# Performance work log

Measured on AMD Instinct MI355X. Metric: run time of the kernel, lower is better.

## Reference

```python
import jax, jax.numpy as jnp
import numpy as np

NEG_BIG = 1e8  # mask value from the original code


def setup_inputs() -> dict:
    key = jax.random.key(0)
    k1, k2, k3, k4, k5 = jax.random.split(key, 5)
    B, L, H, D = 16, 128, 256, 256
    # xavier-uniform-ish scale for the weight matrices
    lim = float(np.sqrt(6.0 / (H + D)))
    return {
        "encoder_output": jax.random.normal(k1, (B, L, H), dtype=jnp.float32),
        "W_l": jax.random.uniform(k2, (H, D), jnp.float32, -lim, lim),
        "W_r": jax.random.uniform(k3, (H, D), jnp.float32, -lim, lim),
        "U": jax.random.uniform(k4, (D,), jnp.float32, 0.0, 1.0),
        "logit_bias": jax.random.uniform(k5, (1,), jnp.float32, 0.0, 1.0),
    }


def reference(encoder_output, W_l, W_r, U, logit_bias):
    B, L, H = encoder_output.shape
    # projections: (B, L, D)
    dot_l = jnp.einsum("blh,hd->bld", encoder_output, W_l)
    dot_r = jnp.einsum("blh,hd->bld", encoder_output, W_r)
    # pairwise additive attention: (B, L, L, D) -> (B, L, L)
    final_sum = jnp.tanh(dot_l[:, :, None, :] + dot_r[:, None, :, :])
    logits = jnp.einsum("bijd,d->bij", final_sum, U) + logit_bias[0]
    # per-step diagonal mask (one_hot(i) at step i) vectorized as eye
    mask = jnp.eye(L, dtype=logits.dtype)  # (L, L)
    mask_scores = logits - NEG_BIG * mask[None, :, :]  # (B, L, L)
    probs = jax.nn.sigmoid(mask_scores)
    # Bernoulli sample (fixed key for reproducibility)
    samples = jax.random.bernoulli(jax.random.key(1), probs).astype(logits.dtype)  # graphs (B,L,L)
    # Bernoulli entropy: p*softplus(-l) + (1-p)*softplus(l), numerically stable
    entropy = probs * jax.nn.softplus(-mask_scores) + (1.0 - probs) * jax.nn.softplus(mask_scores)
    graph_batch = jnp.mean(samples, axis=0)  # (L, L)
    # BCE-with-logits mean over all elements (targets = sampled graphs)
    log_softmax = jnp.mean(jax.nn.softplus(mask_scores) - mask_scores * samples)
    entropy_regularization = jnp.mean(jnp.mean(entropy, axis=2), axis=1)  # (B,)
    return (mask_scores, samples, entropy, graph_batch, log_softmax, entropy_regularization)
```

## Files before the change

### kernel.cpp

```cpp
#include <hip/hip_runtime.h>

#define Bn 16
#define Ln 128
#define Hn 256
#define Dn 256

#define OFF_MASK   0
#define OFF_SMP    262144
#define OFF_ENT    524288
#define OFF_GRAPH  786432
#define OFF_LSE    802816
#define OFF_EREG   802817

static __device__ __forceinline__ unsigned rotl32(unsigned x, int r) {
  return (x << r) | (x >> (32 - r));
}

static __device__ __forceinline__ unsigned threefry_bits(unsigned c_hi, unsigned c_lo) {
  const unsigned ks0 = 0u, ks1 = 1u;
  const unsigned ks2 = 0u ^ 1u ^ 0x1BD11BDAu;
  unsigned x0 = c_hi + ks0;
  unsigned x1 = c_lo + ks1;
  x0 += x1; x1 = rotl32(x1, 13); x1 ^= x0;
  x0 += x1; x1 = rotl32(x1, 15); x1 ^= x0;
  x0 += x1; x1 = rotl32(x1, 26); x1 ^= x0;
  x0 += x1; x1 = rotl32(x1, 6);  x1 ^= x0;
  x0 += ks1; x1 += ks2 + 1u;
  x0 += x1; x1 = rotl32(x1, 17); x1 ^= x0;
  x0 += x1; x1 = rotl32(x1, 29); x1 ^= x0;
  x0 += x1; x1 = rotl32(x1, 16); x1 ^= x0;
  x0 += x1; x1 = rotl32(x1, 24); x1 ^= x0;
  x0 += ks2; x1 += ks0 + 2u;
  x0 += x1; x1 = rotl32(x1, 13); x1 ^= x0;
  x0 += x1; x1 = rotl32(x1, 15); x1 ^= x0;
  x0 += x1; x1 = rotl32(x1, 26); x1 ^= x0;
  x0 += x1; x1 = rotl32(x1, 6);  x1 ^= x0;
  x0 += ks0; x1 += ks1 + 3u;
  x0 += x1; x1 = rotl32(x1, 17); x1 ^= x0;
  x0 += x1; x1 = rotl32(x1, 29); x1 ^= x0;
  x0 += x1; x1 = rotl32(x1, 16); x1 ^= x0;
  x0 += x1; x1 = rotl32(x1, 24); x1 ^= x0;
  x0 += ks1; x1 += ks2 + 4u;
  x0 += x1; x1 = rotl32(x1, 13); x1 ^= x0;
  x0 += x1; x1 = rotl32(x1, 15); x1 ^= x0;
  x0 += x1; x1 = rotl32(x1, 26); x1 ^= x0;
  x0 += x1; x1 = rotl32(x1, 6);  x1 ^= x0;
  x0 += ks2; x1 += ks0 + 5u;
  return x0 ^ x1;
}

static __device__ __forceinline__ float softplus_f(float x) {
  return fmaxf(x, 0.0f) + log1pf(__expf(-fabsf(x)));
}

static __device__ __forceinline__ float fast_tanh(float x) {
  float e = __expf(-2.0f * x);
  float r = __builtin_amdgcn_rcpf(1.0f + e);
  return fmaf(2.0f, r, -1.0f);
}

__global__ void proj_kernel(const float* __restrict__ enc,
                            const float* __restrict__ Wl,
                            const float* __restrict__ Wr,
                            float* __restrict__ dl,
                            float* __restrict__ dr,
                            float* __restrict__ out,
                            double* __restrict__ ws_acc) {
  int gid = blockIdx.x * blockDim.x + threadIdx.x;
  if (gid < Ln * Ln) out[OFF_GRAPH + gid] = 0.0f;
  if (gid < 17) ws_acc[gid] = 0.0;

  int r0 = blockIdx.x * 4;
  int d = threadIdx.x;
  __shared__ float encS[4][Hn];
  ((float4*)encS)[d] = ((const float4*)(enc + (size_t)r0 * Hn))[d];
  __syncthreads();

  float al[4] = {0.f, 0.f, 0.f, 0.f};
  float ar[4] = {0.f, 0.f, 0.f, 0.f};
  for (int h4 = 0; h4 < Hn / 4; ++h4) {
    float4 e[4];
#pragma unroll
    for (int r = 0; r < 4; ++r) e[r] = ((const float4*)encS[r])[h4];
#pragma unroll
    for (int q = 0; q < 4; ++q) {
      int h = h4 * 4 + q;
      float wl = Wl[h * Dn + d];
      float wr = Wr[h * Dn + d];
#pragma unroll
      for (int r = 0; r < 4; ++r) {
        float ev = (q == 0) ? e[r].x : (q == 1) ? e[r].y : (q == 2) ? e[r].z : e[r].w;
        al[r] = fmaf(ev, wl, al[r]);
        ar[r] = fmaf(ev, wr, ar[r]);
      }
    }
  }
#pragma unroll
  for (int r = 0; r < 4; ++r) {
    dl[(size_t)(r0 + r) * Dn + d] = al[r];
    dr[(size_t)(r0 + r) * Dn + d] = ar[r];
  }
}

__global__ void pair_kernel(const float* __restrict__ dl,
                            const float* __restrict__ dr,
                            const float* __restrict__ U,
                            const float* __restrict__ bias,
                            float* __restrict__ out,
                            double* __restrict__ ws_acc) {
  int blk = blockIdx.x;
  int b = blk >> 5;
  int i0 = (blk & 31) * 4;
  int t = threadIdx.x;
  int dp = t & 15;
  int jj = t >> 4;

  __shared__ float pS[4][8 * 256];
  __shared__ float redS[8];

  float dlr[4][16], Ur[16];
  {
    const float4* U4 = (const float4*)(U + dp * 16);
#pragma unroll
    for (int q = 0; q < 4; ++q) {
      float4 u = U4[q];
      Ur[4*q+0] = u.x; Ur[4*q+1] = u.y; Ur[4*q+2] = u.z; Ur[4*q+3] = u.w;
    }
#pragma unroll
    for (int r = 0; r < 4; ++r) {
      const float4* dl4 = (const float4*)(dl + (size_t)(b * Ln + i0 + r) * Dn + dp * 16);
#pragma unroll
      for (int q = 0; q < 4; ++q) {
        float4 a = dl4[q];
        dlr[r][4*q+0] = a.x; dlr[r][4*q+1] = a.y; dlr[r][4*q+2] = a.z; dlr[r][4*q+3] = a.w;
      }
    }
  }

  const float* drt = dr + (size_t)b * Ln * Dn + (size_t)jj * Dn + dp * 16;
#pragma unroll
  for (int tl = 0; tl < 8; ++tl) {
    const float4* drp = (const float4*)(drt + (size_t)tl * 16 * Dn);
    float a0 = 0.f, a1 = 0.f, a2 = 0.f, a3 = 0.f;
#pragma unroll
    for (int q = 0; q < 4; ++q) {
      float4 v = drp[q];
#pragma unroll
      for (int c = 0; c < 4; ++c) {
        float dv = (c == 0) ? v.x : (c == 1) ? v.y : (c == 2) ? v.z : v.w;
        float uv = Ur[4*q+c];
        a0 = fmaf(fast_tanh(dlr[0][4*q+c] + dv), uv, a0);
        a1 = fmaf(fast_tanh(dlr[1][4*q+c] + dv), uv, a1);
        a2 = fmaf(fast_tanh(dlr[2][4*q+c] + dv), uv, a2);
        a3 = fmaf(fast_tanh(dlr[3][4*q+c] + dv), uv, a3);
      }
    }
    int sa = tl * 256 + jj * 16 + dp;
    pS[0][sa] = a0; pS[1][sa] = a1; pS[2][sa] = a2; pS[3][sa] = a3;
  }
  __syncthreads();

  float ent_v = 0.0f, lse_v = 0.0f;
  int j = t & 127;
#pragma unroll
  for (int rr = 0; rr < 2; ++rr) {
    int row = rr * 2 + (t >> 7);
    const float* ps = &pS[row][(j >> 4) * 256 + (j & 15) * 16];
    float tot = 0.0f;
#pragma unroll
    for (int k = 0; k < 16; ++k) tot += ps[k];
    int i = i0 + row;
    float l = tot + bias[0] - ((j == i) ? 1.0e8f : 0.0f);
    float e = __expf(-l);
    float p = __builtin_amdgcn_rcpf(1.0f + e);
    unsigned n = ((unsigned)(b * Ln + i) << 7) | (unsigned)j;
    unsigned bits = threefry_bits(0u, n);
    float u = __uint_as_float((bits >> 9) | 0x3f800000u) - 1.0f;
    float smp = (u < p) ? 1.0f : 0.0f;
    float sp_pos = softplus_f(l);
    float sp_neg = softplus_f(-l);
    float ent = p * sp_neg + (1.0f - p) * sp_pos;
    size_t idx = (size_t)(b * Ln + i) * Ln + j;
    out[OFF_MASK + idx] = l;
    out[OFF_SMP + idx] = smp;
    out[OFF_ENT + idx] = ent;
    atomicAdd(&out[OFF_GRAPH + i * Ln + j], smp * 0.0625f);
    ent_v += ent;
    lse_v += sp_pos - l * smp;
  }

#pragma unroll
  for (int off = 32; off > 0; off >>= 1) {
    ent_v += __shfl_down(ent_v, off);
    lse_v += __shfl_down(lse_v, off);
  }
  if ((t & 63) == 0) {
    redS[(t >> 6) * 2 + 0] = ent_v;
    redS[(t >> 6) * 2 + 1] = lse_v;
  }
  __syncthreads();
  if (t == 0) {
    float es = redS[0] + redS[2] + redS[4] + redS[6];
    float ls = redS[1] + redS[3] + redS[5] + redS[7];
    atomicAdd(&ws_acc[b], (double)es);
    atomicAdd(&ws_acc[16], (double)ls);
  }
}

__global__ void finalize_kernel(const double* __restrict__ ws_acc, float* __restrict__ out) {
  int t = threadIdx.x;
  if (t == 0) out[OFF_LSE] = (float)(ws_acc[16] / (double)(Bn * Ln * Ln));
  if (t < Bn) out[OFF_EREG + t] = (float)(ws_acc[t] / (double)(Ln * Ln));
}

extern "C" void kernel_launch(void* const* d_in, const int* in_sizes, int n_in,
                              void* d_out, int out_size, void* d_ws, size_t ws_size,
                              hipStream_t stream) {
  const float* enc = (const float*)d_in[0];
  const float* Wl = (const float*)d_in[1];
  const float* Wr = (const float*)d_in[2];
  const float* U = (const float*)d_in[3];
  const float* bias = (const float*)d_in[4];
  float* out = (float*)d_out;

  float* dl = (float*)d_ws;
  float* dr = dl + (size_t)Bn * Ln * Dn;
  double* ws_acc = (double*)(dr + (size_t)Bn * Ln * Dn);

  proj_kernel<<<Bn * Ln / 4, 256, 0, stream>>>(enc, Wl, Wr, dl, dr, out, ws_acc);
  pair_kernel<<<Bn * Ln / 4, 256, 0, stream>>>(dl, dr, U, bias, out, ws_acc);
  finalize_kernel<<<1, 64, 0, stream>>>(ws_acc, out);
}
```

Baseline: 112.8 us.

## Fuse projection, pairwise and finalize kernels into one cooperative grid-synced kernel

Replaces the three separate launches with a single cooperative kernel that separates the projection, pairwise-logit and finalize phases with grid-wide syncs. Each block keeps its own four rows of the left projection in shared memory, so dl is no longer written to or re-read from global memory. The aim is to remove inter-kernel launch gaps and some global traffic. In exchange it adds grid-sync overhead and needs all 512 blocks to be resident at once, which launch_bounds(256,2) and the shared-memory footprint have to allow.

Result: slower. 221.5 us (+96.4%).

```diff
diff --git a/kernel.cpp b/kernel.cpp
--- a/kernel.cpp
+++ b/kernel.cpp
@@ -1,4 +1,7 @@
 #include <hip/hip_runtime.h>
+#include <hip/hip_cooperative_groups.h>
+
+namespace cg = cooperative_groups;
 
 #define Bn 16
 #define Ln 128
@@ -59,64 +62,66 @@
   return fmaf(2.0f, r, -1.0f);
 }
 
-__global__ void proj_kernel(const float* __restrict__ enc,
-                            const float* __restrict__ Wl,
-                            const float* __restrict__ Wr,
-                            float* __restrict__ dl,
-                            float* __restrict__ dr,
-                            float* __restrict__ out,
-                            double* __restrict__ ws_acc) {
-  int gid = blockIdx.x * blockDim.x + threadIdx.x;
-  if (gid < Ln * Ln) out[OFF_GRAPH + gid] = 0.0f;
-  if (gid < 17) ws_acc[gid] = 0.0;
-
-  int r0 = blockIdx.x * 4;
-  int d = threadIdx.x;
+__global__ __launch_bounds__(256, 2) void fused_kernel(
+    const float* __restrict__ enc,
+    const float* __restrict__ Wl,
+    const float* __restrict__ Wr,
+    const float* __restrict__ U,
+    const float* __restrict__ bias,
+    float* __restrict__ dr,
+    float* __restrict__ out,
+    double* __restrict__ ws_acc) {
+  cg::grid_group grid = cg::this_grid();
+  int blk = blockIdx.x;
+  int t = threadIdx.x;
+
+  __shared__ float dlS[4][Dn];
   __shared__ float encS[4][Hn];
-  ((float4*)encS)[d] = ((const float4*)(enc + (size_t)r0 * Hn))[d];
-  __syncthreads();
-
-  float al[4] = {0.f, 0.f, 0.f, 0.f};
-  float ar[4] = {0.f, 0.f, 0.f, 0.f};
-  for (int h4 = 0; h4 < Hn / 4; ++h4) {
-    float4 e[4];
-#pragma unroll
-    for (int r = 0; r < 4; ++r) e[r] = ((const float4*)encS[r])[h4];
-#pragma unroll
-    for (int q = 0; q < 4; ++q) {
-      int h = h4 * 4 + q;
-      float wl = Wl[h * Dn + d];
-      float wr = Wr[h * Dn + d];
-#pragma unroll
-      for (int r = 0; r < 4; ++r) {
-        float ev = (q == 0) ? e[r].x : (q == 1) ? e[r].y : (q == 2) ? e[r].z : e[r].w;
-        al[r] = fmaf(ev, wl, al[r]);
-        ar[r] = fmaf(ev, wr, ar[r]);
+  __shared__ float pS[4][8 * 256];
+  __shared__ float redS[8];
+
+  {
+    int gid = blk * 256 + t;
+    if (gid < Ln * Ln) out[OFF_GRAPH + gid] = 0.0f;
+    if (gid < 17) ws_acc[gid] = 0.0;
+
+    int r0 = blk * 4;
+    int d = t;
+    ((float4*)encS)[d] = ((const float4*)(enc + (size_t)r0 * Hn))[d];
+    __syncthreads();
+
+    float al[4] = {0.f, 0.f, 0.f, 0.f};
+    float ar[4] = {0.f, 0.f, 0.f, 0.f};
+    for (int h4 = 0; h4 < Hn / 4; ++h4) {
+      float4 e[4];
+#pragma unroll
+      for (int r = 0; r < 4; ++r) e[r] = ((const float4*)encS[r])[h4];
+#pragma unroll
+      for (int q = 0; q < 4; ++q) {
+        int h = h4 * 4 + q;
+        float wl = Wl[h * Dn + d];
+        float wr = Wr[h * Dn + d];
+#pragma unroll
+        for (int r = 0; r < 4; ++r) {
+          float ev = (q == 0) ? e[r].x : (q == 1) ? e[r].y : (q == 2) ? e[r].z : e[r].w;
+          al[r] = fmaf(ev, wl, al[r]);
+          ar[r] = fmaf(ev, wr, ar[r]);
+        }
       }
     }
-  }
-#pragma unroll
-  for (int r = 0; r < 4; ++r) {
-    dl[(size_t)(r0 + r) * Dn + d] = al[r];
-    dr[(size_t)(r0 + r) * Dn + d] = ar[r];
-  }
-}
-
-__global__ void pair_kernel(const float* __restrict__ dl,
-                            const float* __restrict__ dr,
-                            const float* __restrict__ U,
-                            const float* __restrict__ bias,
-                            float* __restrict__ out,
-                            double* __restrict__ ws_acc) {
-  int blk = blockIdx.x;
+#pragma unroll
+    for (int r = 0; r < 4; ++r) {
+      dlS[r][d] = al[r];
+      dr[(size_t)(r0 + r) * Dn + d] = ar[r];
+    }
+  }
+
+  grid.sync();
+
   int b = blk >> 5;
   int i0 = (blk & 31) * 4;
-  int t = threadIdx.x;
   int dp = t & 15;
   int jj = t >> 4;
-
-  __shared__ float pS[4][8 * 256];
-  __shared__ float redS[8];
 
   float dlr[4][16], Ur[16];
   {
@@ -128,10 +133,9 @@
     }
 #pragma unroll
     for (int r = 0; r < 4; ++r) {
-      const float4* dl4 = (const float4*)(dl + (size_t)(b * Ln + i0 + r) * Dn + dp * 16);
 #pragma unroll
       for (int q = 0; q < 4; ++q) {
-        float4 a = dl4[q];
+        float4 a = *(const float4*)&dlS[r][dp * 16 + q * 4];
         dlr[r][4*q+0] = a.x; dlr[r][4*q+1] = a.y; dlr[r][4*q+2] = a.z; dlr[r][4*q+3] = a.w;
       }
     }
@@ -205,12 +209,13 @@
     atomicAdd(&ws_acc[b], (double)es);
     atomicAdd(&ws_acc[16], (double)ls);
   }
-}
-
-__global__ void finalize_kernel(const double* __restrict__ ws_acc, float* __restrict__ out) {
-  int t = threadIdx.x;
-  if (t == 0) out[OFF_LSE] = (float)(ws_acc[16] / (double)(Bn * Ln * Ln));
-  if (t < Bn) out[OFF_EREG + t] = (float)(ws_acc[t] / (double)(Ln * Ln));
+
+  grid.sync();
+
+  if (blk == 0) {
+    if (t == 0) out[OFF_LSE] = (float)(ws_acc[16] / (double)(Bn * Ln * Ln));
+    if (t < Bn) out[OFF_EREG + t] = (float)(ws_acc[t] / (double)(Ln * Ln));
+  }
 }
 
 extern "C" void kernel_launch(void* const* d_in, const int* in_sizes, int n_in,
@@ -223,11 +228,11 @@
   const float* bias = (const float*)d_in[4];
   float* out = (float*)d_out;
 
-  float* dl = (float*)d_ws;
-  float* dr = dl + (size_t)Bn * Ln * Dn;
+  float* dr = (float*)d_ws;
   double* ws_acc = (double*)(dr + (size_t)Bn * Ln * Dn);
 
-  proj_kernel<<<Bn * Ln / 4, 256, 0, stream>>>(enc, Wl, Wr, dl, dr, out, ws_acc);
-  pair_kernel<<<Bn * Ln / 4, 256, 0, stream>>>(dl, dr, U, bias, out, ws_acc);
-  finalize_kernel<<<1, 64, 0, stream>>>(ws_acc, out);
-}
+  void* kargs[] = {(void*)&enc, (void*)&Wl, (void*)&Wr, (void*)&U,
+                   (void*)&bias, (void*)&dr, (void*)&out, (void*)&ws_acc};
+  hipLaunchCooperativeKernel((void*)fused_kernel, dim3(Bn * Ln / 4), dim3(256),
+                             kargs, 0, stream);
+}
```
